# Kernel tuning notes

Measured on AMD Instinct MI355X. Metric: run time of the kernel, lower is better.

Reference implementation:

```python
import jax, jax.numpy as jnp
import numpy as np

P, U, R, C = 100000, 20000, 1000, 500
D, T, B = 64, 50, 4096
ET = 50000
NNZ_COL, NNZ_REG, NNZ_CAT, NNZ_T = 1_000_000, 300_000, 300_000, 1_000_000
N_LAYERS = 2


def setup_inputs() -> dict:
    key = jax.random.key(0)
    ks = iter(jax.random.split(key, 64))
    def nrm(shape, s=0.05):
        return (jax.random.normal(next(ks), shape, jnp.float32) * s)
    def ridx(n, hi):
        return jax.random.randint(next(ks), (n,), 0, hi, dtype=jnp.int32)
    def vals(n, scale):
        # roughly degree-normalized positive incidence weights
        return jax.random.uniform(next(ks), (n,), jnp.float32) * scale
    inp = {
        'user_idx': ridx(B, U),
        'user_seq': ridx((B, T)[0] * T, P + 1).reshape(B, T),
        'user_seq_mask': jax.random.randint(next(ks), (B, T), 0, 2, dtype=jnp.int32),
        'col_poi_idx': ridx(NNZ_COL, P), 'col_user_idx': ridx(NNZ_COL, U),
        'col_vals_pe': vals(NNZ_COL, 0.02), 'col_vals_ep': vals(NNZ_COL, 0.1),
        'reg_poi_idx': ridx(NNZ_REG, P), 'reg_region_idx': ridx(NNZ_REG, R),
        'reg_vals_pe': vals(NNZ_REG, 0.005), 'reg_vals_ep': vals(NNZ_REG, 0.3),
        'cat_poi_idx': ridx(NNZ_CAT, P), 'cat_cat_idx': ridx(NNZ_CAT, C),
        'cat_vals_pe': vals(NNZ_CAT, 0.003), 'cat_vals_ep': vals(NNZ_CAT, 0.3),
        'trans_poi_idx': ridx(NNZ_T, P), 'trans_edge_idx': ridx(NNZ_T, ET),
        'trans_vals_tar': vals(NNZ_T, 0.05), 'trans_vals_src': vals(NNZ_T, 0.1),
        'poi_emb': nrm((P + 1, D)), 'user_emb': nrm((U, D)),
        'region_emb': nrm((R, D)), 'cat_emb': nrm((C, D)),
        'w_gate_col': nrm((D, D)), 'b_gate_col': nrm((1, D)),
        'w_gate_trans': nrm((D, D)), 'b_gate_trans': nrm((1, D)),
        'w_gate_reg': nrm((D, D)), 'b_gate_reg': nrm((1, D)),
        'w_gate_cat': nrm((D, D)), 'b_gate_cat': nrm((1, D)),
        'col_Wp': nrm((D, D)), 'col_We': nrm((D, D)), 'col_Wf': nrm((2 * D, D)),
        'reg_Wp': nrm((D, D)), 'reg_We': nrm((D, D)), 'reg_Wf': nrm((2 * D, D)),
        'cat_Wp': nrm((D, D)), 'cat_We': nrm((D, D)), 'cat_Wf': nrm((2 * D, D)),
    }
    return inp


def _spmm(rows, cols, vals, X, n_rows):
    # sparse[n_rows, n_cols] @ X : gather source rows, scale, scatter-add to dest
    return jax.ops.segment_sum(vals[:, None] * X[cols], rows, num_segments=n_rows)


def _gate(x, W, b):
    return x * jax.nn.sigmoid(x @ W + b)


def _hetero_net(poi, edge, poi_idx, edge_idx, vals_pe, vals_ep, Wp, We, Wf, n_edge):
    # HG_poi_to_edge: rows=edge_idx, cols=poi_idx ; HG_edge_to_poi: rows=poi_idx, cols=edge_idx
    n_poi = poi.shape[0]
    acc_p, acc_e = poi, edge
    p, e = poi, edge
    for _ in range(N_LAYERS):
        poi_msg = _spmm(edge_idx, poi_idx, vals_pe, p @ Wp, n_edge)   # [n_edge, D]
        fused = jnp.concatenate([poi_msg, e @ We], axis=1) @ Wf       # [n_edge, D]
        prop = _spmm(poi_idx, edge_idx, vals_ep, fused, n_poi)        # [n_poi, D]
        p = prop + p      # residual (dropout p=0 -> identity)
        e = fused + e
        acc_p = acc_p + p
        acc_e = acc_e + e
    inv = 1.0 / (N_LAYERS + 1)
    return acc_p * inv, acc_e * inv


def _directed_net(poi, poi_idx, edge_idx, vals_tar, vals_src):
    n_poi = poi.shape[0]
    acc = poi
    p = poi
    for _ in range(N_LAYERS):
        msg_tar = _spmm(edge_idx, poi_idx, vals_tar, p, ET)       # HG_poi_tar @ p
        msg_src = _spmm(poi_idx, edge_idx, vals_src, msg_tar, n_poi)  # HG_poi_src @ msg_tar
        p = msg_src + p
        acc = acc + p
    return acc / (N_LAYERS + 1)


def _masked_mean(seq_embs, mask):
    m = mask.astype(seq_embs.dtype)[..., None]  # [B,T,1]
    denom = jnp.clip(m.sum(axis=1), 1.0)
    return (seq_embs * m).sum(axis=1) / denom


def reference(user_idx, user_seq, user_seq_mask,
              col_poi_idx, col_user_idx, col_vals_pe, col_vals_ep,
              reg_poi_idx, reg_region_idx, reg_vals_pe, reg_vals_ep,
              cat_poi_idx, cat_cat_idx, cat_vals_pe, cat_vals_ep,
              trans_poi_idx, trans_edge_idx, trans_vals_tar, trans_vals_src,
              poi_emb, user_emb, region_emb, cat_emb,
              w_gate_col, b_gate_col, w_gate_trans, b_gate_trans,
              w_gate_reg, b_gate_reg, w_gate_cat, b_gate_cat,
              col_Wp, col_We, col_Wf, reg_Wp, reg_We, reg_Wf,
              cat_Wp, cat_We, cat_Wf):
    base = poi_emb[:-1]  # drop padding row, [P, D]
    col_p = _gate(base, w_gate_col, b_gate_col)
    trans_p = _gate(base, w_gate_trans, b_gate_trans)
    reg_p = _gate(base, w_gate_reg, b_gate_reg)
    cat_p = _gate(base, w_gate_cat, b_gate_cat)

    col_poi_out, col_user_out = _hetero_net(col_p, user_emb, col_poi_idx, col_user_idx,
                                            col_vals_pe, col_vals_ep, col_Wp, col_We, col_Wf, U)
    reg_poi_out, _ = _hetero_net(reg_p, region_emb, reg_poi_idx, reg_region_idx,
                                 reg_vals_pe, reg_vals_ep, reg_Wp, reg_We, reg_Wf, R)
    cat_poi_out, _ = _hetero_net(cat_p, cat_emb, cat_poi_idx, cat_cat_idx,
                                 cat_vals_pe, cat_vals_ep, cat_Wp, cat_We, cat_Wf, C)
    trans_poi_out = _directed_net(trans_p, trans_poi_idx, trans_edge_idx,
                                  trans_vals_tar, trans_vals_src)

    zero = jnp.zeros((1, D), base.dtype)
    col_pad = jnp.concatenate([col_poi_out, zero], axis=0)
    reg_pad = jnp.concatenate([reg_poi_out, zero], axis=0)
    cat_pad = jnp.concatenate([cat_poi_out, zero], axis=0)
    trans_pad = jnp.concatenate([trans_poi_out, zero], axis=0)

    col_u = col_user_out[user_idx] + _masked_mean(col_pad[user_seq], user_seq_mask)
    reg_u = _masked_mean(reg_pad[user_seq], user_seq_mask)
    cat_u = _masked_mean(cat_pad[user_seq], user_seq_mask)
    trans_u = _masked_mean(trans_pad[user_seq], user_seq_mask)

    return jnp.stack([col_u, trans_u, reg_u, cat_u])  # [4, B, D]


if __name__ == '__main__':
    out = reference(**setup_inputs())
    print(out.shape, out.dtype)
```

## Files before the change

### kernel.cpp

```cpp
#include <hip/hip_runtime.h>

#define D 64
constexpr int Pn  = 100000;
constexpr int Un  = 20000;
constexpr int Rn  = 1000;
constexpr int Cn  = 500;
constexpr int Tn  = 50;
constexpr int Bn  = 4096;
constexpr int ETn = 50000;
constexpr int NNZ_COL = 1000000;
constexpr int NNZ_REG = 300000;
constexpr int NNZ_CAT = 300000;
constexpr int NNZ_T   = 1000000;
constexpr int TILE = 16384;
constexpr int CAP2 = 1536;
constexpr int NB2  = (Pn + 127) / 128;

static inline int cdiv(int a, int b) { return (a + b - 1) / b; }

__device__ __forceinline__ unsigned short f2bf(float f) {
  unsigned u = __float_as_uint(f);
  unsigned r = (u + 0x7FFF + ((u >> 16) & 1)) >> 16;
  return (unsigned short)r;
}
__device__ __forceinline__ float bflo(unsigned d) {
  return __uint_as_float(d << 16);
}
__device__ __forceinline__ float bfhi(unsigned d) {
  return __uint_as_float(d & 0xFFFF0000u);
}
__device__ __forceinline__ unsigned packbf(float a, float b) {
  return (unsigned)f2bf(a) | ((unsigned)f2bf(b) << 16);
}

struct SG {
  const int* k1; const int* o1; const float* v1;
  const int* k2; const int* o2; const float* v2;
  int2* sd; int* rowptr; int* cursorB;
  int s1, nb1, nk1, cap1, nblk, nnz, tile0, bkt0;
};
struct SG4 { SG g[4]; };

__global__ __launch_bounds__(256) void gate_kernel(
    const float* __restrict__ Xin, const float* __restrict__ W,
    const float* __restrict__ bias, unsigned short* __restrict__ P16,
    unsigned short* __restrict__ A16, int N) {
  __shared__ float sx[4][D];
  int tid = threadIdx.x, wv = tid >> 6, lane = tid & 63;
  float wcol[D];
#pragma unroll
  for (int k = 0; k < D; ++k) wcol[k] = W[k * D + lane];
  float bl = bias[lane];
  for (int row = blockIdx.x * 4 + wv; row < N; row += gridDim.x * 4) {
    float x = Xin[row * D + lane];
    sx[wv][lane] = x;
    float y = 0.f;
#pragma unroll
    for (int k = 0; k < D; ++k) y += sx[wv][k] * wcol[k];
    float s = 1.f / (1.f + __expf(-(y + bl)));
    float o = x * s;
    unsigned short ob = f2bf(o);
    P16[row * D + lane] = ob;
    A16[row * D + lane] = ob;
  }
}

__global__ __launch_bounds__(256) void matmul_kernel(
    const float* __restrict__ Xin, const float* __restrict__ W,
    float* __restrict__ Y, int N) {
  __shared__ float sx[4][D];
  int tid = threadIdx.x, wv = tid >> 6, lane = tid & 63;
  float wcol[D];
#pragma unroll
  for (int k = 0; k < D; ++k) wcol[k] = W[k * D + lane];
  for (int row = blockIdx.x * 4 + wv; row < N; row += gridDim.x * 4) {
    sx[wv][lane] = Xin[row * D + lane];
    float y = 0.f;
#pragma unroll
    for (int k = 0; k < D; ++k) y += sx[wv][k] * wcol[k];
    Y[row * D + lane] = y;
  }
}

__global__ __launch_bounds__(256) void fused2_resid_kernel(
    const float* __restrict__ A, const float* __restrict__ W1,
    const float* __restrict__ W2, unsigned short* __restrict__ fusedOut16,
    float* __restrict__ e_buf, float* __restrict__ accE, int N) {
  __shared__ float sa[4][D], sb2[4][D];
  int tid = threadIdx.x, wv = tid >> 6, lane = tid & 63;
  float w1[D], w2[D];
#pragma unroll
  for (int k = 0; k < D; ++k) {
    w1[k] = W1[k * D + lane];
    w2[k] = W2[k * D + lane];
  }
  for (int row = blockIdx.x * 4 + wv; row < N; row += gridDim.x * 4) {
    sa[wv][lane]  = A[row * D + lane];
    float eo = e_buf[row * D + lane];
    sb2[wv][lane] = eo;
    float y = 0.f;
#pragma unroll
    for (int k = 0; k < D; ++k) y += sa[wv][k] * w1[k] + sb2[wv][k] * w2[k];
    fusedOut16[row * D + lane] = f2bf(y);
    float en = eo + y;
    e_buf[row * D + lane] = en;
    accE[row * D + lane] += en;
  }
}

__global__ __launch_bounds__(256) void cursor_init_b_kernel(SG4 gs, int totb) {
  int b = blockIdx.x * blockDim.x + threadIdx.x;
  if (b >= totb) return;
  int gi = 3;
  while (gi > 0 && b < gs.g[gi].bkt0) --gi;
  const SG& g = gs.g[gi];
  int lb = b - g.bkt0;
  g.cursorB[lb] =
      (lb < g.nb1) ? lb * g.cap1 : g.nb1 * g.cap1 + (lb - g.nb1) * CAP2;
}

__global__ __launch_bounds__(1024) void scatter_b_kernel(SG4 gs) {
  extern __shared__ int ls[];
  int b = blockIdx.x;
  int gi = 3;
  while (gi > 0 && b < gs.g[gi].tile0) --gi;
  const SG& g = gs.g[gi];
  int t = b - g.tile0;
  bool d2 = t >= g.nblk;
  const int* kk = d2 ? g.k2 : g.k1;
  const int* oo = d2 ? g.o2 : g.o1;
  const float* vv = d2 ? g.v2 : g.v1;
  int sft = d2 ? 7 : g.s1;
  int kb = d2 ? g.nb1 : 0;
  int nb = d2 ? NB2 : g.nb1;
  int msk = (1 << sft) - 1;
  int tile = d2 ? t - g.nblk : t;
  int* cnt = ls;
  int* bas = ls + nb;
  int tid = threadIdx.x;
  for (int k = tid; k < nb; k += 1024) cnt[k] = 0;
  __syncthreads();
  int t0 = tile * TILE, t1 = min(t0 + TILE, g.nnz);
  for (int i = t0 + tid; i < t1; i += 1024) atomicAdd(&cnt[kk[i] >> sft], 1);
  __syncthreads();
  for (int k = tid; k < nb; k += 1024) {
    int c = cnt[k];
    bas[k] = c ? atomicAdd(&g.cursorB[kb + k], c) : 0;
  }
  __syncthreads();
  for (int k = tid; k < nb; k += 1024) cnt[k] = 0;
  __syncthreads();
  for (int i = t0 + tid; i < t1; i += 1024) {
    int r = kk[i], key = r >> sft;
    int off = atomicAdd(&cnt[key], 1);
    g.sd[bas[key] + off] =
        make_int2(((r & msk) << 17) | oo[i], __float_as_int(vv[i]));
  }
}

__global__ __launch_bounds__(256) void refine_b_kernel(SG4 gs) {
  __shared__ int cnt[128];
  __shared__ int wsum[2];
  int bg = blockIdx.x;
  int gi = 3;
  while (gi > 0 && bg < gs.g[gi].bkt0) --gi;
  const SG& g = gs.g[gi];
  int b = bg - g.bkt0;
  int tid = threadIdx.x;
  int sft, row0, kbase, klim, bstart;
  if (b < g.nb1) {
    sft = g.s1; row0 = b << g.s1; kbase = 0; klim = g.nk1;
    bstart = b * g.cap1;
  } else {
    sft = 7; row0 = (b - g.nb1) << 7; kbase = g.nk1; klim = Pn;
    bstart = g.nb1 * g.cap1 + (b - g.nb1) * CAP2;
  }
  int rows = min(1 << sft, klim - row0);
  int bend = g.cursorB[b];
  if (rows == 1) {
    if (tid == 0) g.rowptr[kbase + row0] = bstart;
    return;
  }
  if (tid < rows) cnt[tid] = 0;
  __syncthreads();
  int2 st[8];
#pragma unroll
  for (int j = 0; j < 8; ++j) {
    int i = bstart + tid + (j << 8);
    st[j] = (i < bend) ? g.sd[i] : make_int2(0, 0);
  }
#pragma unroll
  for (int j = 0; j < 8; ++j) {
    int i = bstart + tid + (j << 8);
    if (i < bend) atomicAdd(&cnt[st[j].x >> 17], 1);
  }
  __syncthreads();
  int v = 0, sc = 0;
  if (tid < 128) {
    v = (tid < rows) ? cnt[tid] : 0;
    sc = v;
    int lane = tid & 63;
#pragma unroll
    for (int d = 1; d < 64; d <<= 1) {
      int y = __shfl_up(sc, d);
      if (lane >= d) sc += y;
    }
    if (lane == 63) wsum[tid >> 6] = sc;
  }
  __syncthreads();
  int excl = sc - v + ((tid >= 64 && tid < 128) ? wsum[0] : 0);
  __syncthreads();
  if (tid < rows) {
    g.rowptr[kbase + row0 + tid] = bstart + excl;
    cnt[tid] = excl;
  }
  __syncthreads();
#pragma unroll
  for (int j = 0; j < 8; ++j) {
    int i = bstart + tid + (j << 8);
    if (i < bend) {
      int r = st[j].x >> 17;
      int dst = bstart + atomicAdd(&cnt[r], 1);
      g.sd[dst] = st[j];
    }
  }
}

__global__ __launch_bounds__(256) void spmm_csr_kernel(
    const int* __restrict__ rowptr, const int* __restrict__ bEnd, int base,
    int nkx, int sft, int boff, const int2* __restrict__ sd,
    const uint4* __restrict__ X128, float* __restrict__ Yf,
    uint4* __restrict__ Y128, uint4* __restrict__ p128,
    uint4* __restrict__ a128, int nrows) {
  int lane = threadIdx.x & 63;
  int q = lane >> 3, l3 = lane & 7;
  int w = (int)((blockIdx.x * (long)blockDim.x + threadIdx.x) >> 6);
  if (w >= nrows) return;
  int idx = base + w;
  int start = rowptr[idx];
  int be = bEnd[boff + (w >> sft)];
  int end = (idx + 1 < nkx) ? min(rowptr[idx + 1], be) : be;
  float a0 = 0.f, a1 = 0.f, a2 = 0.f, a3 = 0.f;
  float a4 = 0.f, a5 = 0.f, a6 = 0.f, a7 = 0.f;
  float b0 = 0.f, b1 = 0.f, b2 = 0.f, b3 = 0.f;
  float b4 = 0.f, b5 = 0.f, b6 = 0.f, b7 = 0.f;
  int n = start + q;
  for (; n + 8 < end; n += 16) {
    int2 c0 = sd[n], c1 = sd[n + 8];
    uint4 d0 = X128[(size_t)(c0.x & 0x1FFFF) * 8 + l3];
    uint4 d1 = X128[(size_t)(c1.x & 0x1FFFF) * 8 + l3];
    float v0 = __int_as_float(c0.y), v1 = __int_as_float(c1.y);
    a0 += v0 * bflo(d0.x); a1 += v0 * bfhi(d0.x);
    a2 += v0 * bflo(d0.y); a3 += v0 * bfhi(d0.y);
    a4 += v0 * bflo(d0.z); a5 += v0 * bfhi(d0.z);
    a6 += v0 * bflo(d0.w); a7 += v0 * bfhi(d0.w);
    b0 += v1 * bflo(d1.x); b1 += v1 * bfhi(d1.x);
    b2 += v1 * bflo(d1.y); b3 += v1 * bfhi(d1.y);
    b4 += v1 * bflo(d1.z); b5 += v1 * bfhi(d1.z);
    b6 += v1 * bflo(d1.w); b7 += v1 * bfhi(d1.w);
  }
  for (; n < end; n += 8) {
    int2 cv = sd[n];
    uint4 dv = X128[(size_t)(cv.x & 0x1FFFF) * 8 + l3];
    float v = __int_as_float(cv.y);
    a0 += v * bflo(dv.x); a1 += v * bfhi(dv.x);
    a2 += v * bflo(dv.y); a3 += v * bfhi(dv.y);
    a4 += v * bflo(dv.z); a5 += v * bfhi(dv.z);
    a6 += v * bflo(dv.w); a7 += v * bfhi(dv.w);
  }
  float y0 = a0 + b0, y1 = a1 + b1, y2 = a2 + b2, y3 = a3 + b3;
  float y4 = a4 + b4, y5 = a5 + b5, y6 = a6 + b6, y7 = a7 + b7;
#pragma unroll
  for (int m = 8; m <= 32; m <<= 1) {
    y0 += __shfl(y0, lane ^ m); y1 += __shfl(y1, lane ^ m);
    y2 += __shfl(y2, lane ^ m); y3 += __shfl(y3, lane ^ m);
    y4 += __shfl(y4, lane ^ m); y5 += __shfl(y5, lane ^ m);
    y6 += __shfl(y6, lane ^ m); y7 += __shfl(y7, lane ^ m);
  }
  if (lane >= 8) return;
  size_t o = (size_t)w * 8 + l3;
  if (p128) {
    uint4 pv = p128[o];
    float p0 = bflo(pv.x) + y0, p1 = bfhi(pv.x) + y1;
    float p2 = bflo(pv.y) + y2, p3 = bfhi(pv.y) + y3;
    float p4 = bflo(pv.z) + y4, p5 = bfhi(pv.z) + y5;
    float p6 = bflo(pv.w) + y6, p7 = bfhi(pv.w) + y7;
    uint4 pn;
    pn.x = packbf(p0, p1); pn.y = packbf(p2, p3);
    pn.z = packbf(p4, p5); pn.w = packbf(p6, p7);
    p128[o] = pn;
    uint4 av = a128[o];
    uint4 an;
    an.x = packbf(bflo(av.x) + p0, bfhi(av.x) + p1);
    an.y = packbf(bflo(av.y) + p2, bfhi(av.y) + p3);
    an.z = packbf(bflo(av.z) + p4, bfhi(av.z) + p5);
    an.w = packbf(bflo(av.w) + p6, bfhi(av.w) + p7);
    a128[o] = an;
  } else if (Y128) {
    uint4 pk;
    pk.x = packbf(y0, y1); pk.y = packbf(y2, y3);
    pk.z = packbf(y4, y5); pk.w = packbf(y6, y7);
    Y128[o] = pk;
  } else {
    float4 lo; lo.x = y0; lo.y = y1; lo.z = y2; lo.w = y3;
    float4 hi; hi.x = y4; hi.y = y5; hi.z = y6; hi.w = y7;
    *(float4*)&Yf[(size_t)w * D + 8 * l3] = lo;
    *(float4*)&Yf[(size_t)w * D + 8 * l3 + 4] = hi;
  }
}

__global__ __launch_bounds__(256) void copy2_kernel(
    const float4* __restrict__ s, float4* __restrict__ a,
    float4* __restrict__ b, int n4) {
  int i = blockIdx.x * blockDim.x + threadIdx.x;
  if (i < n4) {
    float4 v = s[i];
    a[i] = v;
    b[i] = v;
  }
}

__global__ __launch_bounds__(256) void final_kernel(
    const int* __restrict__ user_idx, const int* __restrict__ seq,
    const int* __restrict__ mask, const uint2* __restrict__ colP16,
    const uint2* __restrict__ transP16, const uint2* __restrict__ regP16,
    const uint2* __restrict__ catP16, const float* __restrict__ colU,
    float* __restrict__ out) {
  int lane = threadIdx.x & 63;
  int q = lane >> 4, l4 = lane & 15;
  int wid = (int)((blockIdx.x * (long)blockDim.x + threadIdx.x) >> 6);
  if (wid >= Bn) return;
  float c0 = 0.f, c1 = 0.f, c2 = 0.f, c3 = 0.f;
  float t0 = 0.f, t1 = 0.f, t2 = 0.f, t3 = 0.f;
  float r0 = 0.f, r1 = 0.f, r2 = 0.f, r3 = 0.f;
  float g0 = 0.f, g1 = 0.f, g2 = 0.f, g3 = 0.f;
  int cnt = 0;
  for (int t = q; t < Tn; t += 4) {
    int m = mask[wid * Tn + t];
    int idx = seq[wid * Tn + t];
    cnt += m;
    if (m && idx < Pn) {
      size_t ro = (size_t)idx * 16 + l4;
      uint2 dc = colP16[ro];
      uint2 dt = transP16[ro];
      uint2 dr = regP16[ro];
      uint2 dg = catP16[ro];
      c0 += bflo(dc.x); c1 += bfhi(dc.x); c2 += bflo(dc.y); c3 += bfhi(dc.y);
      t0 += bflo(dt.x); t1 += bfhi(dt.x); t2 += bflo(dt.y); t3 += bfhi(dt.y);
      r0 += bflo(dr.x); r1 += bfhi(dr.x); r2 += bflo(dr.y); r3 += bfhi(dr.y);
      g0 += bflo(dg.x); g1 += bfhi(dg.x); g2 += bflo(dg.y); g3 += bfhi(dg.y);
    }
  }
  cnt += __shfl(cnt, lane ^ 16); cnt += __shfl(cnt, lane ^ 32);
  c0 += __shfl(c0, lane ^ 16); c0 += __shfl(c0, lane ^ 32);
  c1 += __shfl(c1, lane ^ 16); c1 += __shfl(c1, lane ^ 32);
  c2 += __shfl(c2, lane ^ 16); c2 += __shfl(c2, lane ^ 32);
  c3 += __shfl(c3, lane ^ 16); c3 += __shfl(c3, lane ^ 32);
  t0 += __shfl(t0, lane ^ 16); t0 += __shfl(t0, lane ^ 32);
  t1 += __shfl(t1, lane ^ 16); t1 += __shfl(t1, lane ^ 32);
  t2 += __shfl(t2, lane ^ 16); t2 += __shfl(t2, lane ^ 32);
  t3 += __shfl(t3, lane ^ 16); t3 += __shfl(t3, lane ^ 32);
  r0 += __shfl(r0, lane ^ 16); r0 += __shfl(r0, lane ^ 32);
  r1 += __shfl(r1, lane ^ 16); r1 += __shfl(r1, lane ^ 32);
  r2 += __shfl(r2, lane ^ 16); r2 += __shfl(r2, lane ^ 32);
  r3 += __shfl(r3, lane ^ 16); r3 += __shfl(r3, lane ^ 32);
  g0 += __shfl(g0, lane ^ 16); g0 += __shfl(g0, lane ^ 32);
  g1 += __shfl(g1, lane ^ 16); g1 += __shfl(g1, lane ^ 32);
  g2 += __shfl(g2, lane ^ 16); g2 += __shfl(g2, lane ^ 32);
  g3 += __shfl(g3, lane ^ 16); g3 += __shfl(g3, lane ^ 32);
  if (lane >= 16) return;
  float dn = 1.f / (float)(cnt > 0 ? cnt : 1);
  const float inv = 1.f / 3.f;
  int u = user_idx[wid];
  float4 cu = *(const float4*)&colU[(size_t)u * D + 4 * l4];
  size_t ob = (size_t)wid * D + 4 * l4;
  float4 o0;
  o0.x = (cu.x + c0 * dn) * inv; o0.y = (cu.y + c1 * dn) * inv;
  o0.z = (cu.z + c2 * dn) * inv; o0.w = (cu.w + c3 * dn) * inv;
  *(float4*)&out[0 * Bn * D + ob] = o0;
  float4 o1v;
  o1v.x = t0 * dn * inv; o1v.y = t1 * dn * inv;
  o1v.z = t2 * dn * inv; o1v.w = t3 * dn * inv;
  *(float4*)&out[1 * Bn * D + ob] = o1v;
  float4 o2v;
  o2v.x = r0 * dn * inv; o2v.y = r1 * dn * inv;
  o2v.z = r2 * dn * inv; o2v.w = r3 * dn * inv;
  *(float4*)&out[2 * Bn * D + ob] = o2v;
  float4 o3v;
  o3v.x = g0 * dn * inv; o3v.y = g1 * dn * inv;
  o3v.z = g2 * dn * inv; o3v.w = g3 * dn * inv;
  *(float4*)&out[3 * Bn * D + ob] = o3v;
}

extern "C" void kernel_launch(void* const* d_in, const int* in_sizes, int n_in,
                              void* d_out, int out_size, void* d_ws,
                              size_t ws_size, hipStream_t stream) {
  (void)in_sizes; (void)n_in; (void)out_size; (void)ws_size;
  const int*   user_idx      = (const int*)d_in[0];
  const int*   user_seq      = (const int*)d_in[1];
  const int*   user_seq_mask = (const int*)d_in[2];
  const int*   col_poi_idx   = (const int*)d_in[3];
  const int*   col_user_idx  = (const int*)d_in[4];
  const float* col_vals_pe   = (const float*)d_in[5];
  const float* col_vals_ep   = (const float*)d_in[6];
  const int*   reg_poi_idx   = (const int*)d_in[7];
  const int*   reg_region_idx= (const int*)d_in[8];
  const float* reg_vals_pe   = (const float*)d_in[9];
  const float* reg_vals_ep   = (const float*)d_in[10];
  const int*   cat_poi_idx   = (const int*)d_in[11];
  const int*   cat_cat_idx   = (const int*)d_in[12];
  const float* cat_vals_pe   = (const float*)d_in[13];
  const float* cat_vals_ep   = (const float*)d_in[14];
  const int*   trans_poi_idx = (const int*)d_in[15];
  const int*   trans_edge_idx= (const int*)d_in[16];
  const float* trans_vals_tar= (const float*)d_in[17];
  const float* trans_vals_src= (const float*)d_in[18];
  const float* poi_emb       = (const float*)d_in[19];
  const float* user_emb      = (const float*)d_in[20];
  const float* region_emb    = (const float*)d_in[21];
  const float* cat_emb       = (const float*)d_in[22];
  const float* w_gate_col    = (const float*)d_in[23];
  const float* b_gate_col    = (const float*)d_in[24];
  const float* w_gate_trans  = (const float*)d_in[25];
  const float* b_gate_trans  = (const float*)d_in[26];
  const float* w_gate_reg    = (const float*)d_in[27];
  const float* b_gate_reg    = (const float*)d_in[28];
  const float* w_gate_cat    = (const float*)d_in[29];
  const float* b_gate_cat    = (const float*)d_in[30];
  const float* col_Wp = (const float*)d_in[31];
  const float* col_We = (const float*)d_in[32];
  const float* col_Wf = (const float*)d_in[33];
  const float* reg_Wp = (const float*)d_in[34];
  const float* reg_We = (const float*)d_in[35];
  const float* reg_Wf = (const float*)d_in[36];
  const float* cat_Wp = (const float*)d_in[37];
  const float* cat_We = (const float*)d_in[38];
  const float* cat_Wf = (const float*)d_in[39];

  float* ws = (float*)d_ws;
  size_t off = 0;
  auto alloc = [&](size_t n) { float* p = ws + off; off += n; return p; };
  const size_t PD = (size_t)Pn * D;
  const size_t UD = (size_t)Un * D;
  const size_t ED = (size_t)ETn * D;

  float* colU   = alloc(UD);
  float* e_buf  = alloc(UD);
  float* tmpE1  = alloc(UD);
  float* acce   = alloc((size_t)Rn * D);
  float* WpWf   = alloc(D * D);
  float* WeWf   = alloc(D * D);
  unsigned short* tmpE2_16 = (unsigned short*)alloc(UD / 2);
  unsigned short* tmpE1_16 = (unsigned short*)alloc(ED / 2);
  unsigned short* p16      = (unsigned short*)alloc(PD / 2);
  unsigned short* colP16   = (unsigned short*)alloc(PD / 2);
  unsigned short* regP16   = (unsigned short*)alloc(PD / 2);
  unsigned short* catP16   = (unsigned short*)alloc(PD / 2);
  unsigned short* transP16 = (unsigned short*)alloc(PD / 2);

  const int s1_[4]   = {5, 0, 0, 6};
  const int nk1_[4]  = {Un, Rn, Cn, ETn};
  const int cap1_[4] = {2048, 512, 1024, 1536};
  const int nnz_[4]  = {NNZ_COL, NNZ_REG, NNZ_CAT, NNZ_T};
  SG4 gs;
  int tile0 = 0, bkt0 = 0;
  size_t sdoff = 0, rpoff = 0;
  int2* sdbase;
  int *rpbase, *curbase;
  {
    size_t sdtot = 0;
    for (int i = 0; i < 4; ++i) {
      int nb1 = cdiv(nk1_[i], 1 << s1_[i]);
      sdtot += (size_t)nb1 * cap1_[i] + (size_t)NB2 * CAP2;
    }
    sdbase = (int2*)alloc(2 * sdtot);
    rpbase = (int*)alloc(Un + Rn + Cn + ETn + 4 * Pn + 8);
    curbase = (int*)alloc(4 * 2048);
  }
  const int* k1s[4] = {col_user_idx, reg_region_idx, cat_cat_idx,
                       trans_edge_idx};
  const int* o1s[4] = {col_poi_idx, reg_poi_idx, cat_poi_idx, trans_poi_idx};
  const float* v1s[4] = {col_vals_pe, reg_vals_pe, cat_vals_pe,
                         trans_vals_tar};
  const float* v2s[4] = {col_vals_ep, reg_vals_ep, cat_vals_ep,
                         trans_vals_src};
  for (int i = 0; i < 4; ++i) {
    SG& g = gs.g[i];
    g.k1 = k1s[i]; g.o1 = o1s[i]; g.v1 = v1s[i];
    g.k2 = o1s[i]; g.o2 = k1s[i]; g.v2 = v2s[i];
    g.s1 = s1_[i]; g.nk1 = nk1_[i]; g.cap1 = cap1_[i]; g.nnz = nnz_[i];
    g.nb1 = cdiv(g.nk1, 1 << g.s1);
    g.nblk = cdiv(g.nnz, TILE);
    g.sd = sdbase + sdoff;
    g.rowptr = rpbase + rpoff;
    g.cursorB = curbase + i * 2048;
    g.tile0 = tile0; g.bkt0 = bkt0;
    sdoff += (size_t)g.nb1 * g.cap1 + (size_t)NB2 * CAP2;
    rpoff += g.nk1 + Pn;
    tile0 += 2 * g.nblk;
    bkt0 += g.nb1 + NB2;
  }
  int tottiles = tile0, totbkt = bkt0;

  cursor_init_b_kernel<<<cdiv(totbkt, 256), 256, 0, stream>>>(gs, totbkt);
  scatter_b_kernel<<<tottiles, 1024, 8192, stream>>>(gs);
  refine_b_kernel<<<totbkt, 256, 0, stream>>>(gs);

  const int GCAP = 1024;

  auto spmm = [&](const SG& g, int base, int sft, int boff,
                  const unsigned short* X16, float* Yf, unsigned short* Y16,
                  unsigned short* prmw, unsigned short* armw, int nrows) {
    spmm_csr_kernel<<<cdiv(nrows, 4), 256, 0, stream>>>(
        g.rowptr, g.cursorB, base, g.nk1 + Pn, sft, boff, g.sd,
        (const uint4*)X16, Yf, (uint4*)Y16, (uint4*)prmw, (uint4*)armw,
        nrows);
  };

  auto hetero = [&](int gi, const float* wg, const float* bg,
                    const float* edge_emb, int Ne, const float* Wp,
                    const float* We, const float* Wf, float* accE,
                    unsigned short* acc16) {
    const SG& g = gs.g[gi];
    gate_kernel<<<GCAP, 256, 0, stream>>>(poi_emb, wg, bg, p16, acc16, Pn);
    copy2_kernel<<<cdiv(Ne * D / 4, 256), 256, 0, stream>>>(
        (const float4*)edge_emb, (float4*)e_buf, (float4*)accE, Ne * D / 4);
    matmul_kernel<<<16, 256, 0, stream>>>(Wp, Wf, WpWf, D);
    matmul_kernel<<<16, 256, 0, stream>>>(We, Wf + D * D, WeWf, D);
    for (int l = 0; l < 2; ++l) {
      spmm(g, 0, g.s1, 0, p16, tmpE1, nullptr, nullptr, nullptr, Ne);
      fused2_resid_kernel<<<min(cdiv(Ne, 4), GCAP), 256, 0, stream>>>(
          tmpE1, WpWf, WeWf, tmpE2_16, e_buf, accE, Ne);
      spmm(g, g.nk1, 7, g.nb1, tmpE2_16, nullptr, nullptr, p16, acc16, Pn);
    }
  };

  hetero(0, w_gate_col, b_gate_col, user_emb, Un, col_Wp, col_We, col_Wf,
         colU, colP16);
  hetero(1, w_gate_reg, b_gate_reg, region_emb, Rn, reg_Wp, reg_We, reg_Wf,
         acce, regP16);
  hetero(2, w_gate_cat, b_gate_cat, cat_emb, Cn, cat_Wp, cat_We, cat_Wf,
         acce, catP16);

  {
    const SG& g = gs.g[3];
    gate_kernel<<<GCAP, 256, 0, stream>>>(poi_emb, w_gate_trans, b_gate_trans,
                                          p16, transP16, Pn);
    for (int l = 0; l < 2; ++l) {
      spmm(g, 0, g.s1, 0, p16, nullptr, tmpE1_16, nullptr, nullptr, ETn);
      spmm(g, g.nk1, 7, g.nb1, tmpE1_16, nullptr, nullptr, p16, transP16, Pn);
    }
  }

  final_kernel<<<cdiv(Bn * 64, 256), 256, 0, stream>>>(
      user_idx, user_seq, user_seq_mask, (const uint2*)colP16,
      (const uint2*)transP16, (const uint2*)regP16, (const uint2*)catP16,
      colU, (float*)d_out);
}
```

Before: 776.9 us.

## Stage bucketed scatter in LDS for contiguous global writes

The bucket scatter kernel now keeps each tile's entries in registers, computes per-bucket offsets with a block-wide prefix scan, and stages the entries bucket-sorted in shared memory. It then writes them out linearly, using a binary search over bucket bases, so that global stores within a bucket are contiguous instead of scattered. The tile size drops to fit the staging buffer in LDS, which means more blocks and more global cursor atomics. The extra passes also add synchronisations and per-element search work. Correctness relies on nb being at most 1024.

```diff
diff --git a/kernel.cpp b/kernel.cpp
--- a/kernel.cpp
+++ b/kernel.cpp
@@ -12,7 +12,8 @@
 constexpr int NNZ_REG = 300000;
 constexpr int NNZ_CAT = 300000;
 constexpr int NNZ_T   = 1000000;
-constexpr int TILE = 16384;
+constexpr int STILE = 7040;
+constexpr int NBMAX = 1024;
 constexpr int CAP2 = 1536;
 constexpr int NB2  = (Pn + 127) / 128;
 
@@ -121,6 +122,11 @@
 
 __global__ __launch_bounds__(1024) void scatter_b_kernel(SG4 gs) {
   extern __shared__ int ls[];
+  int2* stage = (int2*)ls;
+  int* lcnt   = ls;
+  int* lbase  = ls + 2 * STILE;
+  int* gbase  = lbase + (NBMAX + 1);
+  __shared__ int wsum[17];
   int b = blockIdx.x;
   int gi = 3;
   while (gi > 0 && b < gs.g[gi].tile0) --gi;
@@ -135,26 +141,66 @@
   int nb = d2 ? NB2 : g.nb1;
   int msk = (1 << sft) - 1;
   int tile = d2 ? t - g.nblk : t;
-  int* cnt = ls;
-  int* bas = ls + nb;
   int tid = threadIdx.x;
-  for (int k = tid; k < nb; k += 1024) cnt[k] = 0;
-  __syncthreads();
-  int t0 = tile * TILE, t1 = min(t0 + TILE, g.nnz);
-  for (int i = t0 + tid; i < t1; i += 1024) atomicAdd(&cnt[kk[i] >> sft], 1);
-  __syncthreads();
-  for (int k = tid; k < nb; k += 1024) {
-    int c = cnt[k];
-    bas[k] = c ? atomicAdd(&g.cursorB[kb + k], c) : 0;
-  }
-  __syncthreads();
-  for (int k = tid; k < nb; k += 1024) cnt[k] = 0;
-  __syncthreads();
-  for (int i = t0 + tid; i < t1; i += 1024) {
-    int r = kk[i], key = r >> sft;
-    int off = atomicAdd(&cnt[key], 1);
-    g.sd[bas[key] + off] =
-        make_int2(((r & msk) << 17) | oo[i], __float_as_int(vv[i]));
+  for (int k = tid; k < nb; k += 1024) lcnt[k] = 0;
+  __syncthreads();
+  int t0 = tile * STILE, t1 = min(t0 + STILE, g.nnz);
+  int fill = t1 - t0;
+  int key[7], off[7], ox[7], vx[7];
+#pragma unroll
+  for (int j = 0; j < 7; ++j) {
+    int i = t0 + j * 1024 + tid;
+    if (i < t1) {
+      int r = kk[i];
+      key[j] = r >> sft;
+      ox[j] = ((r & msk) << 17) | oo[i];
+      vx[j] = __float_as_int(vv[i]);
+      off[j] = atomicAdd(&lcnt[key[j]], 1);
+    } else {
+      key[j] = -1; off[j] = 0; ox[j] = 0; vx[j] = 0;
+    }
+  }
+  __syncthreads();
+  {
+    int lane = tid & 63, wv = tid >> 6;
+    int c = (tid < nb) ? lcnt[tid] : 0;
+    int sc = c;
+#pragma unroll
+    for (int d = 1; d < 64; d <<= 1) {
+      int y = __shfl_up(sc, d);
+      if (lane >= d) sc += y;
+    }
+    if (lane == 63) wsum[wv] = sc;
+    __syncthreads();
+    if (tid < 16) {
+      int w = wsum[tid];
+#pragma unroll
+      for (int d = 1; d < 16; d <<= 1) {
+        int y = __shfl_up(w, d);
+        if (lane >= d) w += y;
+      }
+      wsum[tid] = w;
+    }
+    __syncthreads();
+    int woff = (wv == 0) ? 0 : wsum[wv - 1];
+    if (tid < nb) {
+      lbase[tid] = woff + sc - c;
+      gbase[tid] = c ? atomicAdd(&g.cursorB[kb + tid], c) : 0;
+    }
+    if (tid == 0) lbase[nb] = fill;
+  }
+  __syncthreads();
+#pragma unroll
+  for (int j = 0; j < 7; ++j)
+    if (key[j] >= 0) stage[lbase[key[j]] + off[j]] = make_int2(ox[j], vx[j]);
+  __syncthreads();
+  for (int i = tid; i < fill; i += 1024) {
+    int lo = 0, hi = nb;
+    while (hi - lo > 1) {
+      int mid = (lo + hi) >> 1;
+      if (lbase[mid] <= i) lo = mid; else hi = mid;
+    }
+    g.sd[gbase[lo] + (i - lbase[lo])] = stage[i];
   }
 }
 
@@ -490,7 +536,7 @@
     g.k2 = o1s[i]; g.o2 = k1s[i]; g.v2 = v2s[i];
     g.s1 = s1_[i]; g.nk1 = nk1_[i]; g.cap1 = cap1_[i]; g.nnz = nnz_[i];
     g.nb1 = cdiv(g.nk1, 1 << g.s1);
-    g.nblk = cdiv(g.nnz, TILE);
+    g.nblk = cdiv(g.nnz, STILE);
     g.sd = sdbase + sdoff;
     g.rowptr = rpbase + rpoff;
     g.cursorB = curbase + i * 2048;
@@ -503,7 +549,8 @@
   int tottiles = tile0, totbkt = bkt0;
 
   cursor_init_b_kernel<<<cdiv(totbkt, 256), 256, 0, stream>>>(gs, totbkt);
-  scatter_b_kernel<<<tottiles, 1024, 8192, stream>>>(gs);
+  scatter_b_kernel<<<tottiles, 1024, (2 * STILE + 2 * NBMAX + 1) * 4,
+                     stream>>>(gs);
   refine_b_kernel<<<totbkt, 256, 0, stream>>>(gs);
 
   const int GCAP = 1024;
```

After: 766.9 us. No clear change (-1.3%).
